# Kernel optimization log

Measured on AMD Instinct MI355X. Metric: run time of the kernel, lower is better.

## Reference

```python
import jax, jax.numpy as jnp
import numpy as np

B, QL, T, H = 32, 1, 2048, 512


def setup_inputs() -> dict:
    key = jax.random.key(0)
    ks = jax.random.split(key, 10)
    n = lambda i, shape, sc=1.0: jax.random.normal(ks[i], shape, dtype=jnp.float32) * sc
    inv = 1.0 / np.sqrt(H)
    return {
        "query": n(0, (B, QL, H)),
        "value": n(1, (B, T, H)),
        "last_attn": jax.random.uniform(ks[2], (B, T), dtype=jnp.float32),
        "conv_w": n(3, (H, 1, 3), 0.1),   # Conv1d weight (out_ch, in_ch=1, k=3)
        "conv_b": n(4, (H,), 0.1),
        "q_w": n(5, (H, H), inv),          # query_proj (no bias)
        "v_w": n(6, (H, H), inv),          # value_proj (no bias)
        "s_w": n(7, (1, H), inv),          # score_proj weight
        "s_b": n(8, (1,), 0.1),            # score_proj bias
        "bias": n(9, (H,), 0.1),           # learned additive bias
    }


def reference(query, value, last_attn, conv_w, conv_b, q_w, v_w, s_w, s_b, bias):
    Tlen = last_attn.shape[1]
    # Conv1d(in=1, out=H, k=3, pad=1) over last_attn, then transpose -> (B, T, H)
    pad = jnp.pad(last_attn, ((0, 0), (1, 1)))
    frames = jnp.stack([pad[:, k:k + Tlen] for k in range(3)], axis=0)  # (3, B, T)
    conv_attn = jnp.einsum('hk,kbt->bth', conv_w[:, 0, :], frames) + conv_b  # (B, T, H)
    q = jnp.einsum('bqh,oh->bqo', query, q_w)   # (B, 1, H)
    v = jnp.einsum('bth,oh->bto', value, v_w)   # (B, T, H)
    e = jnp.tanh(q + v + conv_attn + bias)      # (B, T, H), q broadcasts over T
    score = jnp.einsum('bth,oh->bt', e, s_w) + s_b  # (B, T)
    # smoothing=True branch: sigmoid then L1-normalize
    score = jax.nn.sigmoid(score)
    attn = score / jnp.sum(score, axis=-1, keepdims=True)
    context = jnp.einsum('bt,bth->bh', attn, value)  # bmm(attn[:,None,:], value).squeeze(1)
    return context, attn
```

## Files before the change

kernel.cpp:

```cpp
#include <hip/hip_runtime.h>
#include <math.h>

#define B 32
#define T 2048
#define H 512

#define BT2 32
#define ASTR 520

typedef __attribute__((ext_vector_type(8))) __bf16 bf16x8;
typedef __attribute__((ext_vector_type(4))) __bf16 bf16x4v;
typedef __attribute__((ext_vector_type(4))) float f32x4;
typedef __attribute__((ext_vector_type(4))) float floatx4;

union pack8 { bf16x4v h; uint2 u; };

__global__ __launch_bounds__(256) void k_init(const float* __restrict__ query,
                                              const float* __restrict__ q_w,
                                              const float* __restrict__ bias,
                                              const float* __restrict__ v_w,
                                              float* __restrict__ qpb,
                                              unsigned short* __restrict__ wbf,
                                              float* __restrict__ ctx_num,
                                              float* __restrict__ denom) {
    const int blk = blockIdx.x;
    const int tid = threadIdx.x;

    if (blk >= 288) {
#pragma unroll
        for (int i = 0; i < 16; ++i) {
            const int off = tid * 4 + i * 1024;
            *(f32x4*)(ctx_num + off) = (f32x4){0.f, 0.f, 0.f, 0.f};
        }
        if (tid < B) denom[tid] = 0.f;
        return;
    }
    if (blk >= 256) {
        const int c2 = blk - 256;
        const int wv = tid >> 6;
        const int lane = tid & 63;
        const int srow = (c2 >> 2) * 64 + (c2 & 3) * 16 + (lane & 15);
        const int scol0 = (lane >> 4) * 8;
#pragma unroll
        for (int kk = 0; kk < 4; ++kk) {
            const int k = wv * 4 + kk;
            const float* src = v_w + (size_t)srow * H + k * 32 + scol0;
            f32x4 a0 = *(const f32x4*)src;
            f32x4 a1 = *(const f32x4*)(src + 4);
            pack8 p0, p1;
            p0.h = __builtin_convertvector(a0, bf16x4v);
            p1.h = __builtin_convertvector(a1, bf16x4v);
            uint4 u = {p0.u.x, p0.u.y, p1.u.x, p1.u.y};
            *(uint4*)(wbf + ((size_t)c2 * 16 + k) * 512 + lane * 8) = u;
        }
        return;
    }

    const int b = blk >> 3;
    const int s = blk & 7;
    const int wave = tid >> 6;
    const int lane = tid & 63;

    const float* qb = query + (size_t)b * H + lane * 8;
    float4 q0 = *(const float4*)qb;
    float4 q1 = *(const float4*)(qb + 4);

    const int o0 = s * 64 + wave * 16;
#pragma unroll
    for (int i = 0; i < 16; ++i) {
        const int o = o0 + i;
        const float* wr = q_w + (size_t)o * H + lane * 8;
        float4 w0 = *(const float4*)wr;
        float4 w1 = *(const float4*)(wr + 4);
        float acc = w0.x * q0.x + w0.y * q0.y + w0.z * q0.z + w0.w * q0.w +
                    w1.x * q1.x + w1.y * q1.y + w1.z * q1.z + w1.w * q1.w;
#pragma unroll
        for (int m = 1; m < 64; m <<= 1) acc += __shfl_xor(acc, m);
        if (lane == 0) qpb[b * H + o] = acc + bias[o];
    }
}

__global__ __launch_bounds__(512, 4) void k2_fused(const float* __restrict__ value,
                                                   const unsigned short* __restrict__ wbf,
                                                   const float* __restrict__ la,
                                                   const float* __restrict__ conv_w,
                                                   const float* __restrict__ conv_b,
                                                   const float* __restrict__ s_w,
                                                   const float* __restrict__ qpb,
                                                   const float* __restrict__ s_b,
                                                   float* __restrict__ pre_sg,
                                                   float* __restrict__ ctx_num,
                                                   float* __restrict__ denom) {
    __shared__ __align__(16) unsigned short As[BT2 * ASTR];
    __shared__ float las[BT2 + 2];
    __shared__ float redp[BT2][9];
    __shared__ float sgs[BT2];

    const int t0 = blockIdx.x * BT2;
    const int b  = blockIdx.y;
    const int tid = threadIdx.x;
    const int wave = tid >> 6;
    const int lane = tid & 63;
    const int tx   = lane & 15;
    const int quad = lane >> 4;
    const int wn   = wave * 64;

    if (tid < BT2 + 2) {
        const int t = t0 + tid - 1;
        las[tid] = (t >= 0 && t < T) ? la[b * T + t] : 0.f;
    }

    {
        const int srow = tid >> 4;
        const int scol = (tid & 15) * 8;
        const float* sg = value + ((size_t)b * T + t0 + srow) * H + scol;
        unsigned short* sl = &As[srow * ASTR + scol];
#pragma unroll
        for (int c = 0; c < 4; ++c) {
            f32x4 a0 = *(const f32x4*)(sg + c * 128);
            f32x4 a1 = *(const f32x4*)(sg + c * 128 + 4);
            pack8 p0, p1;
            p0.h = __builtin_convertvector(a0, bf16x4v);
            p1.h = __builtin_convertvector(a1, bf16x4v);
            uint4 u = {p0.u.x, p0.u.y, p1.u.x, p1.u.y};
            *(uint4*)(sl + c * 128) = u;
        }
    }
    __syncthreads();

    floatx4 acc[2][4];
#pragma unroll
    for (int i = 0; i < 2; ++i)
#pragma unroll
        for (int j = 0; j < 4; ++j) acc[i][j] = (floatx4){0.f, 0.f, 0.f, 0.f};

    const unsigned short* gB = wbf + (size_t)wave * 32768 + lane * 8;
    const unsigned short* aB = &As[tx * ASTR + quad * 8];

#pragma unroll 4
    for (int k = 0; k < 16; ++k) {
        bf16x8 bfr[4];
#pragma unroll
        for (int ni = 0; ni < 4; ++ni)
            bfr[ni] = *(const bf16x8*)(gB + ni * 8192 + k * 512);
        bf16x8 af[2];
#pragma unroll
        for (int mi = 0; mi < 2; ++mi)
            af[mi] = *(const bf16x8*)(aB + mi * 16 * ASTR + k * 32);
#pragma unroll
        for (int mi = 0; mi < 2; ++mi)
#pragma unroll
            for (int ni = 0; ni < 4; ++ni)
                acc[mi][ni] = __builtin_amdgcn_mfma_f32_16x16x32_bf16(
                    af[mi], bfr[ni], acc[mi][ni], 0, 0, 0);
    }

    float qp4[4], sw4[4], cb4[4], c04[4], c14[4], c24[4];
#pragma unroll
    for (int ni = 0; ni < 4; ++ni) {
        const int ol = wn + ni * 16 + tx;
        qp4[ni] = qpb[b * H + ol];
        sw4[ni] = s_w[ol];
        cb4[ni] = conv_b[ol];
        c04[ni] = conv_w[ol * 3 + 0];
        c14[ni] = conv_w[ol * 3 + 1];
        c24[ni] = conv_w[ol * 3 + 2];
    }

    float sacc[8];
#pragma unroll
    for (int i = 0; i < 8; ++i) sacc[i] = 0.f;
#pragma unroll
    for (int ni = 0; ni < 4; ++ni) {
#pragma unroll
        for (int mi = 0; mi < 2; ++mi)
#pragma unroll
            for (int r = 0; r < 4; ++r) {
                const int tl = mi * 16 + quad * 4 + r;
                const float conv = c04[ni] * las[tl] + c14[ni] * las[tl + 1] +
                                   c24[ni] * las[tl + 2] + cb4[ni];
                const float x = acc[mi][ni][r] + qp4[ni] + conv;
                const float ex = __expf(2.f * x);
                const float th = 1.f - 2.f * __builtin_amdgcn_rcpf(ex + 1.f);
                sacc[mi * 4 + r] += sw4[ni] * th;
            }
    }
#pragma unroll
    for (int i = 0; i < 8; ++i) {
        float v = sacc[i];
        v += __shfl_xor(v, 1);
        v += __shfl_xor(v, 2);
        v += __shfl_xor(v, 4);
        v += __shfl_xor(v, 8);
        if (tx == 0) redp[(i >> 2) * 16 + quad * 4 + (i & 3)][wave] = v;
    }
    __syncthreads();

    if (tid < BT2) {
        float sc = s_b[0];
#pragma unroll
        for (int w = 0; w < 8; ++w) sc += redp[tid][w];
        const float sg = 1.f / (1.f + __expf(-sc));
        sgs[tid] = sg;
        pre_sg[b * T + t0 + tid] = sg;
        float dsum = sg;
#pragma unroll
        for (int m = 1; m < 32; m <<= 1) dsum += __shfl_xor(dsum, m);
        if (tid == 0) atomicAdd(&denom[b], dsum);
    }
    __syncthreads();

    float* redc = (float*)As;
    const int h4 = (tid & 127) * 4;
    const int tp = tid >> 7;
    f32x4 a = {0.f, 0.f, 0.f, 0.f};
    const float* vb = value + ((size_t)b * T + t0) * H + h4;
    for (int t = tp; t < BT2; t += 4) {
        const float w = sgs[t];
        f32x4 v = *(const f32x4*)(vb + (size_t)t * H);
        a.x += w * v.x; a.y += w * v.y; a.z += w * v.z; a.w += w * v.w;
    }
    *(f32x4*)&redc[tp * 512 + h4] = a;
    __syncthreads();
    if (tid < 128) {
        const int h = tid * 4;
        f32x4 r0 = *(const f32x4*)&redc[0 * 512 + h];
        f32x4 r1 = *(const f32x4*)&redc[1 * 512 + h];
        f32x4 r2 = *(const f32x4*)&redc[2 * 512 + h];
        f32x4 r3 = *(const f32x4*)&redc[3 * 512 + h];
        atomicAdd(&ctx_num[b * H + h + 0], r0.x + r1.x + r2.x + r3.x);
        atomicAdd(&ctx_num[b * H + h + 1], r0.y + r1.y + r2.y + r3.y);
        atomicAdd(&ctx_num[b * H + h + 2], r0.z + r1.z + r2.z + r3.z);
        atomicAdd(&ctx_num[b * H + h + 3], r0.w + r1.w + r2.w + r3.w);
    }
}

__global__ __launch_bounds__(256) void k3_scale(const float* __restrict__ pre_sg,
                                                const float* __restrict__ ctx_num,
                                                const float* __restrict__ denom,
                                                float* __restrict__ attn_out,
                                                float* __restrict__ ctx) {
    const int b = blockIdx.x;
    const int tid = threadIdx.x;
    const float inv = 1.f / denom[b];
#pragma unroll
    for (int i = 0; i < 8; ++i) {
        const int t = tid + i * 256;
        attn_out[b * T + t] = pre_sg[b * T + t] * inv;
    }
#pragma unroll
    for (int i = 0; i < 2; ++i) {
        const int h = tid + i * 256;
        ctx[b * H + h] = ctx_num[b * H + h] * inv;
    }
}

extern "C" void kernel_launch(void* const* d_in, const int* in_sizes, int n_in,
                              void* d_out, int out_size, void* d_ws, size_t ws_size,
                              hipStream_t stream) {
    const float* query  = (const float*)d_in[0];
    const float* value  = (const float*)d_in[1];
    const float* la     = (const float*)d_in[2];
    const float* conv_w = (const float*)d_in[3];
    const float* conv_b = (const float*)d_in[4];
    const float* q_w    = (const float*)d_in[5];
    const float* v_w    = (const float*)d_in[6];
    const float* s_w    = (const float*)d_in[7];
    const float* s_b    = (const float*)d_in[8];
    const float* bias   = (const float*)d_in[9];

    float* out  = (float*)d_out;
    float* ctx  = out;
    float* attn = out + B * H;

    float* qpb     = (float*)d_ws;
    float* pre_sg  = qpb + B * H;
    float* ctx_num = pre_sg + B * T;
    float* denom   = ctx_num + B * H;
    unsigned short* wbf = (unsigned short*)(denom + 64);

    k_init<<<289, 256, 0, stream>>>(query, q_w, bias, v_w, qpb, wbf, ctx_num, denom);

    dim3 g2(T / BT2, B);
    k2_fused<<<g2, 512, 0, stream>>>(value, wbf, la, conv_w, conv_b, s_w, qpb, s_b,
                                     pre_sg, ctx_num, denom);

    k3_scale<<<B, 256, 0, stream>>>(pre_sg, ctx_num, denom, attn, ctx);
}
```

Baseline: 275.0 us.

## Double time tile, reuse staged bf16 values for context, fuse final scale

Raises the time tile per block from 32 to 64 rows, which halves the number of blocks and the atomics per batch and doubles the MFMA work per loaded weight fragment. The context accumulation now reads the bf16 copy of value already staged in shared memory instead of re-reading fp32 value from global memory, at some precision cost. The separate scale kernel is removed: a per-batch done counter picks the last block, which normalizes attn and ctx. The larger tile raises LDS use (about 66KB for the tile plus an 8KB reduction buffer) and register pressure, which may lower occupancy under the 512-thread, 4-block launch bound.

```diff
diff --git a/kernel.cpp b/kernel.cpp
--- a/kernel.cpp
+++ b/kernel.cpp
@@ -5,7 +5,7 @@
 #define T 2048
 #define H 512
 
-#define BT2 32
+#define BT2 64
 #define ASTR 520
 
 typedef __attribute__((ext_vector_type(8))) __bf16 bf16x8;
@@ -22,7 +22,8 @@
                                               float* __restrict__ qpb,
                                               unsigned short* __restrict__ wbf,
                                               float* __restrict__ ctx_num,
-                                              float* __restrict__ denom) {
+                                              float* __restrict__ denom,
+                                              int* __restrict__ done) {
     const int blk = blockIdx.x;
     const int tid = threadIdx.x;
 
@@ -32,7 +33,7 @@
             const int off = tid * 4 + i * 1024;
             *(f32x4*)(ctx_num + off) = (f32x4){0.f, 0.f, 0.f, 0.f};
         }
-        if (tid < B) denom[tid] = 0.f;
+        if (tid < B) { denom[tid] = 0.f; done[tid] = 0; }
         return;
     }
     if (blk >= 256) {
@@ -90,11 +91,16 @@
                                                    const float* __restrict__ s_b,
                                                    float* __restrict__ pre_sg,
                                                    float* __restrict__ ctx_num,
-                                                   float* __restrict__ denom) {
+                                                   float* __restrict__ denom,
+                                                   int* __restrict__ done,
+                                                   float* __restrict__ attn_out,
+                                                   float* __restrict__ ctx) {
     __shared__ __align__(16) unsigned short As[BT2 * ASTR];
     __shared__ float las[BT2 + 2];
     __shared__ float redp[BT2][9];
     __shared__ float sgs[BT2];
+    __shared__ float redc[4][H];
+    __shared__ int lastFlag;
 
     const int t0 = blockIdx.x * BT2;
     const int b  = blockIdx.y;
@@ -111,26 +117,26 @@
     }
 
     {
-        const int srow = tid >> 4;
-        const int scol = (tid & 15) * 8;
+        const int srow = tid >> 3;
+        const int scol = (tid & 7) * 8;
         const float* sg = value + ((size_t)b * T + t0 + srow) * H + scol;
         unsigned short* sl = &As[srow * ASTR + scol];
 #pragma unroll
-        for (int c = 0; c < 4; ++c) {
-            f32x4 a0 = *(const f32x4*)(sg + c * 128);
-            f32x4 a1 = *(const f32x4*)(sg + c * 128 + 4);
+        for (int c = 0; c < 8; ++c) {
+            f32x4 a0 = *(const f32x4*)(sg + c * 64);
+            f32x4 a1 = *(const f32x4*)(sg + c * 64 + 4);
             pack8 p0, p1;
             p0.h = __builtin_convertvector(a0, bf16x4v);
             p1.h = __builtin_convertvector(a1, bf16x4v);
             uint4 u = {p0.u.x, p0.u.y, p1.u.x, p1.u.y};
-            *(uint4*)(sl + c * 128) = u;
-        }
-    }
-    __syncthreads();
-
-    floatx4 acc[2][4];
-#pragma unroll
-    for (int i = 0; i < 2; ++i)
+            *(uint4*)(sl + c * 64) = u;
+        }
+    }
+    __syncthreads();
+
+    floatx4 acc[4][4];
+#pragma unroll
+    for (int i = 0; i < 4; ++i)
 #pragma unroll
         for (int j = 0; j < 4; ++j) acc[i][j] = (floatx4){0.f, 0.f, 0.f, 0.f};
 
@@ -143,12 +149,12 @@
 #pragma unroll
         for (int ni = 0; ni < 4; ++ni)
             bfr[ni] = *(const bf16x8*)(gB + ni * 8192 + k * 512);
-        bf16x8 af[2];
-#pragma unroll
-        for (int mi = 0; mi < 2; ++mi)
+        bf16x8 af[4];
+#pragma unroll
+        for (int mi = 0; mi < 4; ++mi)
             af[mi] = *(const bf16x8*)(aB + mi * 16 * ASTR + k * 32);
 #pragma unroll
-        for (int mi = 0; mi < 2; ++mi)
+        for (int mi = 0; mi < 4; ++mi)
 #pragma unroll
             for (int ni = 0; ni < 4; ++ni)
                 acc[mi][ni] = __builtin_amdgcn_mfma_f32_16x16x32_bf16(
@@ -167,13 +173,13 @@
         c24[ni] = conv_w[ol * 3 + 2];
     }
 
-    float sacc[8];
-#pragma unroll
-    for (int i = 0; i < 8; ++i) sacc[i] = 0.f;
+    float sacc[16];
+#pragma unroll
+    for (int i = 0; i < 16; ++i) sacc[i] = 0.f;
 #pragma unroll
     for (int ni = 0; ni < 4; ++ni) {
 #pragma unroll
-        for (int mi = 0; mi < 2; ++mi)
+        for (int mi = 0; mi < 4; ++mi)
 #pragma unroll
             for (int r = 0; r < 4; ++r) {
                 const int tl = mi * 16 + quad * 4 + r;
@@ -186,7 +192,7 @@
             }
     }
 #pragma unroll
-    for (int i = 0; i < 8; ++i) {
+    for (int i = 0; i < 16; ++i) {
         float v = sacc[i];
         v += __shfl_xor(v, 1);
         v += __shfl_xor(v, 2);
@@ -205,53 +211,57 @@
         pre_sg[b * T + t0 + tid] = sg;
         float dsum = sg;
 #pragma unroll
-        for (int m = 1; m < 32; m <<= 1) dsum += __shfl_xor(dsum, m);
+        for (int m = 1; m < 64; m <<= 1) dsum += __shfl_xor(dsum, m);
         if (tid == 0) atomicAdd(&denom[b], dsum);
     }
     __syncthreads();
 
-    float* redc = (float*)As;
-    const int h4 = (tid & 127) * 4;
-    const int tp = tid >> 7;
-    f32x4 a = {0.f, 0.f, 0.f, 0.f};
-    const float* vb = value + ((size_t)b * T + t0) * H + h4;
-    for (int t = tp; t < BT2; t += 4) {
-        const float w = sgs[t];
-        f32x4 v = *(const f32x4*)(vb + (size_t)t * H);
-        a.x += w * v.x; a.y += w * v.y; a.z += w * v.z; a.w += w * v.w;
-    }
-    *(f32x4*)&redc[tp * 512 + h4] = a;
+    {
+        const int h4 = (tid & 127) * 4;
+        const int tp = tid >> 7;
+        f32x4 a = {0.f, 0.f, 0.f, 0.f};
+        for (int t = tp; t < BT2; t += 4) {
+            const float w = sgs[t];
+            bf16x4v hv = *(const bf16x4v*)&As[t * ASTR + h4];
+            f32x4 v = __builtin_convertvector(hv, f32x4);
+            a.x += w * v.x; a.y += w * v.y; a.z += w * v.z; a.w += w * v.w;
+        }
+        *(f32x4*)&redc[tp][h4] = a;
+    }
     __syncthreads();
     if (tid < 128) {
         const int h = tid * 4;
-        f32x4 r0 = *(const f32x4*)&redc[0 * 512 + h];
-        f32x4 r1 = *(const f32x4*)&redc[1 * 512 + h];
-        f32x4 r2 = *(const f32x4*)&redc[2 * 512 + h];
-        f32x4 r3 = *(const f32x4*)&redc[3 * 512 + h];
+        f32x4 r0 = *(const f32x4*)&redc[0][h];
+        f32x4 r1 = *(const f32x4*)&redc[1][h];
+        f32x4 r2 = *(const f32x4*)&redc[2][h];
+        f32x4 r3 = *(const f32x4*)&redc[3][h];
         atomicAdd(&ctx_num[b * H + h + 0], r0.x + r1.x + r2.x + r3.x);
         atomicAdd(&ctx_num[b * H + h + 1], r0.y + r1.y + r2.y + r3.y);
         atomicAdd(&ctx_num[b * H + h + 2], r0.z + r1.z + r2.z + r3.z);
         atomicAdd(&ctx_num[b * H + h + 3], r0.w + r1.w + r2.w + r3.w);
     }
-}
-
-__global__ __launch_bounds__(256) void k3_scale(const float* __restrict__ pre_sg,
-                                                const float* __restrict__ ctx_num,
-                                                const float* __restrict__ denom,
-                                                float* __restrict__ attn_out,
-                                                float* __restrict__ ctx) {
-    const int b = blockIdx.x;
-    const int tid = threadIdx.x;
-    const float inv = 1.f / denom[b];
-#pragma unroll
-    for (int i = 0; i < 8; ++i) {
-        const int t = tid + i * 256;
-        attn_out[b * T + t] = pre_sg[b * T + t] * inv;
-    }
-#pragma unroll
-    for (int i = 0; i < 2; ++i) {
-        const int h = tid + i * 256;
-        ctx[b * H + h] = ctx_num[b * H + h] * inv;
+
+    __threadfence();
+    if (tid == 0) {
+        const int old = atomicAdd(&done[b], 1);
+        lastFlag = (old == (T / BT2 - 1));
+    }
+    __syncthreads();
+    if (lastFlag) {
+        __threadfence();
+        const float dn = __hip_atomic_load(&denom[b], __ATOMIC_RELAXED,
+                                           __HIP_MEMORY_SCOPE_AGENT);
+        const float inv = 1.f / dn;
+#pragma unroll
+        for (int j = 0; j < 4; ++j) {
+            const int t = tid * 4 + j;
+            const float p = __hip_atomic_load(&pre_sg[b * T + t], __ATOMIC_RELAXED,
+                                              __HIP_MEMORY_SCOPE_AGENT);
+            attn_out[b * T + t] = p * inv;
+        }
+        const float cn = __hip_atomic_load(&ctx_num[b * H + tid], __ATOMIC_RELAXED,
+                                           __HIP_MEMORY_SCOPE_AGENT);
+        ctx[b * H + tid] = cn * inv;
     }
 }
 
@@ -277,13 +287,12 @@
     float* pre_sg  = qpb + B * H;
     float* ctx_num = pre_sg + B * T;
     float* denom   = ctx_num + B * H;
-    unsigned short* wbf = (unsigned short*)(denom + 64);
-
-    k_init<<<289, 256, 0, stream>>>(query, q_w, bias, v_w, qpb, wbf, ctx_num, denom);
+    int*   done    = (int*)(denom + 64);
+    unsigned short* wbf = (unsigned short*)(done + 64);
+
+    k_init<<<289, 256, 0, stream>>>(query, q_w, bias, v_w, qpb, wbf, ctx_num, denom, done);
 
     dim3 g2(T / BT2, B);
     k2_fused<<<g2, 512, 0, stream>>>(value, wbf, la, conv_w, conv_b, s_w, qpb, s_b,
-                                     pre_sg, ctx_num, denom);
-
-    k3_scale<<<B, 256, 0, stream>>>(pre_sg, ctx_num, denom, attn, ctx);
+                                     pre_sg, ctx_num, denom, done, attn, ctx);
 }
```

Result: slower. 413.8 us (+50.5%).
